# Kernel optimization log

Measured on AMD Instinct MI355X. Metric: run time of the kernel, lower is better.

Reference implementation:

```python
import jax, jax.numpy as jnp
import numpy as np

N_KW = 65536
N_DOC = 65536
N = N_KW + N_DOC
D_NODE = 128   # kw_size == middle_dim
D_MID = 128
D_FB = 16
D_T = 8
E = 1048576


def setup_inputs() -> dict:
    key = jax.random.key(0)
    ks = jax.random.split(key, 14)
    X_nodes = jax.random.normal(ks[0], (N, D_NODE), jnp.float32)
    X_feedback = jax.random.normal(ks[1], (N_DOC, D_FB), jnp.float32)
    X_time = jax.random.normal(ks[2], (N_DOC, D_T), jnp.float32)
    src = jax.random.randint(ks[3], (E,), 0, N_KW)            # kw node ids
    dst = N_KW + jax.random.randint(ks[4], (E,), 0, N_DOC)    # doc node ids
    edge_kw2doc = jnp.stack([src, dst])                       # [2, E], row0=src
    edge_doc2kw = jnp.stack([dst, src])

    def lin(k, fan_in, fan_out):
        return jax.random.normal(k, (fan_in, fan_out), jnp.float32) / np.sqrt(fan_in).astype(np.float32)

    params = dict(
        W0=lin(ks[5], D_NODE, D_MID), b0=jnp.zeros((D_MID,), jnp.float32),
        Wg1=lin(ks[6], D_MID, D_MID), bg1=jnp.zeros((D_MID,), jnp.float32),
        Wg2=lin(ks[7], D_MID, D_MID), bg2=jnp.zeros((D_MID,), jnp.float32),
        Wf1=lin(ks[8], D_FB, D_MID), bf1=jnp.zeros((D_MID,), jnp.float32),
        Wf2=lin(ks[9], D_MID, D_MID), bf2=jnp.zeros((D_MID,), jnp.float32),
        Wt1=lin(ks[10], D_T, D_MID), bt1=jnp.zeros((D_MID,), jnp.float32),
        Wt2=lin(ks[11], D_MID, D_MID), bt2=jnp.zeros((D_MID,), jnp.float32),
    )
    return {"X_nodes": X_nodes, "X_feedback": X_feedback, "X_time": X_time,
            "edge_kw2doc": edge_kw2doc, "edge_doc2kw": edge_doc2kw, "n_kw": N_KW, **params}


def _gcn(x, edge, W, b, n):
    # PyG GCNConv: add self-loops, symmetric normalization deg^{-1/2} A deg^{-1/2}, then linear.
    loop = jnp.arange(n)
    srcs = jnp.concatenate([edge[0], loop])
    dsts = jnp.concatenate([edge[1], loop])
    deg = jax.ops.segment_sum(jnp.ones(srcs.shape[0], x.dtype), dsts, num_segments=n)
    dis = jnp.where(deg > 0, jax.lax.rsqrt(jnp.maximum(deg, 1e-12)), jnp.zeros((), x.dtype))
    norm = dis[srcs] * dis[dsts]
    h = x @ W                                   # [N, D_MID]
    msg = h[srcs] * norm[:, None]               # gather on src, [E+N, D_MID]
    return jax.ops.segment_sum(msg, dsts, num_segments=n) + b


def reference(X_nodes, X_feedback, X_time, edge_kw2doc, edge_doc2kw, n_kw,
              W0, b0, Wg1, bg1, Wg2, bg2, Wf1, bf1, Wf2, bf2, Wt1, bt1, Wt2, bt2):
    n = X_nodes.shape[0]
    # feedback / time MLPs (relu on all but last layer)
    xf = jax.nn.relu(X_feedback @ Wf1 + bf1) @ Wf2 + bf2   # [N_DOC, D_MID]
    xt = jax.nn.relu(X_time @ Wt1 + bt1) @ Wt2 + bt2       # [N_DOC, D_MID]
    # layer 0: Linear on kw nodes only; doc rows stay zero
    x = jnp.zeros((n, W0.shape[1]), X_nodes.dtype)
    x = x.at[:n_kw].set(jax.nn.relu(X_nodes[:n_kw] @ W0 + b0))
    # layer 1: GCNConv kw2doc, write doc rows
    x2 = jax.nn.relu(_gcn(x, edge_kw2doc, Wg1, bg1, n))
    x = x.at[n_kw:].set(x2[n_kw:])
    # layer 2: GCNConv doc2kw, write kw rows
    x2 = jax.nn.relu(_gcn(x, edge_doc2kw, Wg2, bg2, n))
    x = x.at[:n_kw].set(x2[:n_kw])
    # merge_f (Mul) then merge_t (Mul) on doc rows
    x = x.at[n_kw:].mul(xf)
    x = x.at[n_kw:].mul(xt)
    return x
```

## Files before the change

kernel.cpp:

```cpp
#include <hip/hip_runtime.h>

#define NKW   65536
#define NDOC  65536
#define NSEG  131072
#define NE    1048576
#define CHUNK 4096
#define NBLK  (NE / CHUNK)

typedef unsigned long long u64;
typedef unsigned short     u16;
typedef unsigned int       u32;
typedef unsigned char      u8;

typedef __attribute__((ext_vector_type(8))) short short8;
typedef __attribute__((ext_vector_type(4))) float f32x4;
typedef __attribute__((ext_vector_type(2))) float f32x2;

union U8 { short8 v; u64 u[2]; short s[8]; };

__device__ __forceinline__ u16 f2bf(float f) {
    u32 u = __builtin_bit_cast(u32, f);
    u = (u + 0x7fffu + ((u >> 16) & 1u)) >> 16;
    return (u16)u;
}
__device__ __forceinline__ float bf2f(u16 h) {
    return __builtin_bit_cast(float, (u32)h << 16);
}
__device__ __forceinline__ u8 f2fp8(float f) {
    u32 pk = __builtin_amdgcn_cvt_pk_fp8_f32(f, f, 0u, false);
    return (u8)pk;
}

#define BUFA_OFF 0ull
#define BUFD_OFF 8388608ull
#define BUFB_OFF 16777216ull
#define BUFC_OFF 33554432ull
#define WF_OFF   50331648ull
#define CSR_OFF  51380224ull
#define CNT_OFF  59768832ull
#define AUX_OFF  60293120ull
#define OFF_OFF  60821504ull
#define DIS_OFF  61345792ull

#define WOFF_W0  0
#define WOFF_WG1 2048
#define WOFF_WG2 4096
#define WOFF_WF1 6144
#define WOFF_WF2 8192
#define WOFF_WT1 10240
#define WOFF_WT2 12288

struct PrepArgs { const float* w[7]; int K[7]; };

__global__ void zero_k(int* __restrict__ p) {
    p[blockIdx.x * 256 + threadIdx.x] = 0;
}

__global__ __launch_bounds__(256) void k1_hist_prep(
        const int* __restrict__ src, const int* __restrict__ dst,
        int* __restrict__ bhist, PrepArgs pa, short8* __restrict__ wfb) {
    __shared__ int h[512];
    const int tid = threadIdx.x;
    if (blockIdx.x < NBLK) {
        for (int i = tid; i < 512; i += 256) h[i] = 0;
        __syncthreads();
        int e0 = blockIdx.x * CHUNK;
        for (int i = tid; i < CHUNK; i += 256) {
            int s = src[e0 + i];
            int d = dst[e0 + i] - NKW;
            atomicAdd(&h[s >> 8], 1);
            atomicAdd(&h[256 + (d >> 8)], 1);
        }
        __syncthreads();
        for (int i = tid; i < 512; i += 256)
            if (h[i]) atomicAdd(&bhist[i], h[i]);
    } else {
        int u = (blockIdx.x - NBLK) * 4 + (tid >> 6);
        if (u < 224) {
            int m = u >> 5, bk = u & 31;
            int kc = bk >> 3, ct = bk & 7;
            int l = tid & 63;
            int K = pa.K[m];
            const float* W = pa.w[m];
            U8 o;
            #pragma unroll
            for (int i = 0; i < 8; ++i) {
                int k   = kc * 32 + 4 * (l >> 4) + (i & 3) + 16 * (i >> 2);
                int col = ct * 16 + (l & 15);
                float v = (k < K) ? W[(size_t)k * 128 + col] : 0.f;
                o.s[i] = (short)f2bf(v);
            }
            wfb[(size_t)m * 2048 + bk * 64 + l] = o.v;
        }
    }
}

__global__ __launch_bounds__(256) void k2_part_gates(
        const int* __restrict__ src, const int* __restrict__ dst,
        const int* __restrict__ bhist, int* __restrict__ bfill,
        u32* __restrict__ pairs,
        const short8* __restrict__ wfb,
        const float* __restrict__ Xfb, const float* __restrict__ Xt,
        const float* __restrict__ bf1v, const float* __restrict__ bf2v,
        const float* __restrict__ bt1v, const float* __restrict__ bt2v,
        u16* __restrict__ g) {
    __shared__ int h[512], sc[512], base[512], gb[512];
    __shared__ u32 staged[2 * CHUNK];
    const int tid = threadIdx.x;

    if (blockIdx.x < NBLK) {
        for (int i = tid; i < 512; i += 256) gb[i] = bhist[i];
        __syncthreads();
        for (int d = 1; d < 512; d <<= 1) {
            int i1 = tid + 256;
            int t0 = (tid >= d) ? gb[tid - d] : 0;
            int t1 = gb[i1 - d];
            __syncthreads();
            gb[tid] += t0; gb[i1] += t1;
            __syncthreads();
        }
        for (int i = tid; i < 512; i += 256) gb[i] -= bhist[i];
        for (int i = tid; i < 512; i += 256) h[i] = 0;
        __syncthreads();

        const int e0 = blockIdx.x * CHUNK;
        int se[16], de[16];
        #pragma unroll
        for (int j = 0; j < 16; ++j) {
            int e = e0 + tid + j * 256;
            se[j] = src[e];
            de[j] = dst[e] - NKW;
            atomicAdd(&h[se[j] >> 8], 1);
            atomicAdd(&h[256 + (de[j] >> 8)], 1);
        }
        __syncthreads();

        sc[tid] = h[tid];
        __syncthreads();
        for (int d = 1; d < 256; d <<= 1) {
            int t = (tid >= d) ? sc[tid - d] : 0;
            __syncthreads();
            sc[tid] += t;
            __syncthreads();
        }
        sc[256 + tid] = h[256 + tid];
        __syncthreads();
        for (int d = 1; d < 256; d <<= 1) {
            int t = (tid >= d) ? sc[256 + tid - d] : 0;
            __syncthreads();
            sc[256 + tid] += t;
            __syncthreads();
        }

        for (int i = tid; i < 512; i += 256) {
            base[i] = gb[i] + atomicAdd(&bfill[i], h[i]);
            sc[i] -= h[i];
            h[i] = 0;
        }
        __syncthreads();

        #pragma unroll
        for (int j = 0; j < 16; ++j) {
            int bk = se[j] >> 8;
            int r  = atomicAdd(&h[bk], 1);
            staged[sc[bk] + r] = ((u32)(se[j] & 255) << 16) | (u32)de[j];
            int bd = 256 + (de[j] >> 8);
            int r2 = atomicAdd(&h[bd], 1);
            staged[CHUNK + sc[bd] + r2] = ((u32)(de[j] & 255) << 16) | (u32)se[j];
        }
        __syncthreads();

        for (int i = tid; i < 512; i += 256) {
            int n = h[i];
            int so = (i < 256 ? 0 : CHUNK) + sc[i];
            u32* dp = pairs + base[i];
            for (int j = 0; j < n; ++j) dp[j] = staged[so + j];
        }
        return;
    }

    u16 (*H)[136] = (u16(*)[136])staged;
    const int w = tid >> 6, l = tid & 63, lr = l & 15, q = l >> 4;
    const int blk  = blockIdx.x - NBLK;
    const int row0 = blk * 64 + w * 16;
    const int lrow = w * 16 + lr;
    const int orow = w * 16 + 4 * q;

    f32x4 acc[8];
    {
        U8 a;
        f32x4 x = *(const f32x4*)(Xfb + (size_t)(row0 + lr) * 16 + 4 * q);
        #pragma unroll
        for (int i = 0; i < 4; ++i) { a.s[i] = (short)f2bf(x[i]); a.s[4 + i] = 0; }
        #pragma unroll
        for (int ct = 0; ct < 8; ++ct)
            acc[ct] = __builtin_amdgcn_mfma_f32_16x16x32_bf16(
                          a.v, wfb[WOFF_WF1 + ct * 64 + l], (f32x4){0.f,0.f,0.f,0.f}, 0, 0, 0);
    }
    #pragma unroll
    for (int ct = 0; ct < 8; ++ct) {
        const int col = ct * 16 + lr;
        const float bb = bf1v[col];
        #pragma unroll
        for (int r = 0; r < 4; ++r)
            H[orow + r][col] = f2bf(fmaxf(acc[ct][r] + bb, 0.f));
    }
    __threadfence_block();

    f32x4 accf[8];
    #pragma unroll
    for (int ct = 0; ct < 8; ++ct) accf[ct] = (f32x4){0.f, 0.f, 0.f, 0.f};
    #pragma unroll
    for (int kc = 0; kc < 4; ++kc) {
        U8 a;
        const int kb = kc * 32 + 4 * q;
        a.u[0] = *(const u64*)&H[lrow][kb];
        a.u[1] = *(const u64*)&H[lrow][kb + 16];
        #pragma unroll
        for (int ct = 0; ct < 8; ++ct)
            accf[ct] = __builtin_amdgcn_mfma_f32_16x16x32_bf16(
                           a.v, wfb[WOFF_WF2 + (kc * 8 + ct) * 64 + l], accf[ct], 0, 0, 0);
    }
    __threadfence_block();

    {
        U8 a;
        #pragma unroll
        for (int i = 0; i < 8; ++i) a.s[i] = 0;
        if (q < 2) {
            f32x4 x = *(const f32x4*)(Xt + (size_t)(row0 + lr) * 8 + 4 * q);
            #pragma unroll
            for (int i = 0; i < 4; ++i) a.s[i] = (short)f2bf(x[i]);
        }
        #pragma unroll
        for (int ct = 0; ct < 8; ++ct)
            acc[ct] = __builtin_amdgcn_mfma_f32_16x16x32_bf16(
                          a.v, wfb[WOFF_WT1 + ct * 64 + l], (f32x4){0.f,0.f,0.f,0.f}, 0, 0, 0);
    }
    #pragma unroll
    for (int ct = 0; ct < 8; ++ct) {
        const int col = ct * 16 + lr;
        const float bb = bt1v[col];
        #pragma unroll
        for (int r = 0; r < 4; ++r)
            H[orow + r][col] = f2bf(fmaxf(acc[ct][r] + bb, 0.f));
    }
    __threadfence_block();

    f32x4 acct[8];
    #pragma unroll
    for (int ct = 0; ct < 8; ++ct) acct[ct] = (f32x4){0.f, 0.f, 0.f, 0.f};
    #pragma unroll
    for (int kc = 0; kc < 4; ++kc) {
        U8 a;
        const int kb = kc * 32 + 4 * q;
        a.u[0] = *(const u64*)&H[lrow][kb];
        a.u[1] = *(const u64*)&H[lrow][kb + 16];
        #pragma unroll
        for (int ct = 0; ct < 8; ++ct)
            acct[ct] = __builtin_amdgcn_mfma_f32_16x16x32_bf16(
                           a.v, wfb[WOFF_WT2 + (kc * 8 + ct) * 64 + l], acct[ct], 0, 0, 0);
    }
    #pragma unroll
    for (int ct = 0; ct < 8; ++ct) {
        const int col = ct * 16 + lr;
        const float b2f = bf2v[col];
        const float b2t = bt2v[col];
        #pragma unroll
        for (int r = 0; r < 4; ++r) {
            float gv = (accf[ct][r] + b2f) * (acct[ct][r] + b2t);
            g[(size_t)(blk * 64 + orow + r) * 128 + col] = f2bf(gv);
        }
    }
}

__global__ __launch_bounds__(256) void k3_build_gemm0(
        const u32* __restrict__ pairs, const int* __restrict__ bhist,
        int* __restrict__ off, int* __restrict__ cnt,
        float* __restrict__ dis, int* __restrict__ csr,
        const float* __restrict__ Xn, const short8* __restrict__ wfb,
        const float* __restrict__ b0, u8* __restrict__ h0f8) {
    __shared__ int lcnt[256], loff[256], bs[256], gsc[512];
    const int tid = threadIdx.x;

    if (blockIdx.x < 512) {
        const int b = blockIdx.x;
        for (int i = tid; i < 512; i += 256) gsc[i] = bhist[i];
        __syncthreads();
        for (int d = 1; d < 512; d <<= 1) {
            int i1 = tid + 256;
            int t0 = (tid >= d) ? gsc[tid - d] : 0;
            int t1 = gsc[i1 - d];
            __syncthreads();
            gsc[tid] += t0; gsc[i1] += t1;
            __syncthreads();
        }
        const int size  = bhist[b];
        const int start = gsc[b] - size;
        lcnt[tid] = 0;
        __syncthreads();
        for (int i = tid; i < size; i += 256)
            atomicAdd(&lcnt[(pairs[start + i] >> 16) & 255], 1);
        __syncthreads();
        int s = lcnt[tid];
        bs[tid] = s;
        __syncthreads();
        for (int d = 1; d < 256; d <<= 1) {
            int t = (tid >= d) ? bs[tid - d] : 0;
            __syncthreads();
            bs[tid] += t;
            __syncthreads();
        }
        const int P = bs[tid] - s;
        const int seg = (b < 256) ? (b * 256 + tid) : (NKW + (b - 256) * 256 + tid);
        off[seg] = start + P;
        cnt[seg] = s;
        dis[seg] = rsqrtf((float)(s + 1));
        loff[tid] = P;
        lcnt[tid] = 0;
        __syncthreads();
        for (int i = tid; i < size; i += 256) {
            u32 p = pairs[start + i];
            int key = (p >> 16) & 255;
            int r = atomicAdd(&lcnt[key], 1);
            csr[start + loff[key] + r] = (int)(p & 0xFFFF);
        }
        return;
    }

    const int blk = blockIdx.x - 512;
    const int w = tid >> 6, l = tid & 63, lr = l & 15, q = l >> 4;
    const int row = blk * 64 + w * 16 + lr;
    f32x4 acc[8];
    #pragma unroll
    for (int ct = 0; ct < 8; ++ct) acc[ct] = (f32x4){0.f, 0.f, 0.f, 0.f};
    #pragma unroll
    for (int kc = 0; kc < 4; ++kc) {
        U8 a;
        const int kb = kc * 32 + 4 * q;
        const float* A = Xn + (size_t)row * 128;
        f32x4 lo = *(const f32x4*)(A + kb);
        f32x4 hi = *(const f32x4*)(A + kb + 16);
        #pragma unroll
        for (int i = 0; i < 4; ++i) {
            a.s[i]     = (short)f2bf(lo[i]);
            a.s[4 + i] = (short)f2bf(hi[i]);
        }
        #pragma unroll
        for (int ct = 0; ct < 8; ++ct)
            acc[ct] = __builtin_amdgcn_mfma_f32_16x16x32_bf16(
                          a.v, wfb[WOFF_W0 + (kc * 8 + ct) * 64 + l], acc[ct], 0, 0, 0);
    }
    const int orow0 = blk * 64 + w * 16 + 4 * q;
    #pragma unroll
    for (int ct = 0; ct < 8; ++ct) {
        const int col = ct * 16 + lr;
        const float bb = b0[col];
        #pragma unroll
        for (int r = 0; r < 4; ++r) {
            float v = fmaxf(acc[ct][r] + bb, 0.f);
            h0f8[(size_t)(orow0 + r) * 128 + col] = f2fp8(v);
        }
    }
}

template<bool KW_SIDE>
__global__ __launch_bounds__(256) void aggf8_k(
        const int* __restrict__ off, const int* __restrict__ cnt,
        const int* __restrict__ csr, const u8* __restrict__ gsrc,
        const u8* __restrict__ h0f8, const float* __restrict__ dis,
        u16* __restrict__ outb) {
    const int r    = blockIdx.x * 16 + (threadIdx.x >> 4);
    const int lane = threadIdx.x & 15;
    const int seg  = KW_SIDE ? r : (NKW + r);
    const int st = off[seg];
    const int n  = cnt[seg];
    float a[8];
    #pragma unroll
    for (int j = 0; j < 8; ++j) a[j] = 0.f;

    #define DECACC(vv) { \
        u32 lo_ = (u32)(vv), hi_ = (u32)((vv) >> 32); \
        f32x2 p0 = __builtin_amdgcn_cvt_pk_f32_fp8(lo_, false); \
        f32x2 p1 = __builtin_amdgcn_cvt_pk_f32_fp8(lo_, true);  \
        f32x2 p2 = __builtin_amdgcn_cvt_pk_f32_fp8(hi_, false); \
        f32x2 p3 = __builtin_amdgcn_cvt_pk_f32_fp8(hi_, true);  \
        a[0] += p0[0]; a[1] += p0[1]; a[2] += p1[0]; a[3] += p1[1]; \
        a[4] += p2[0]; a[5] += p2[1]; a[6] += p3[0]; a[7] += p3[1]; }

    int i = 0;
    for (; i + 8 <= n; i += 8) {
        int nb[8];
        #pragma unroll
        for (int k = 0; k < 8; ++k) nb[k] = csr[st + i + k];
        u64 v[8];
        #pragma unroll
        for (int k = 0; k < 8; ++k)
            v[k] = *(const u64*)(gsrc + (size_t)nb[k] * 128 + lane * 8);
        #pragma unroll
        for (int k = 0; k < 8; ++k) DECACC(v[k])
    }
    for (; i < n; ++i) {
        int nb = csr[st + i];
        u64 v = *(const u64*)(gsrc + (size_t)nb * 128 + lane * 8);
        DECACC(v)
    }
    #undef DECACC

    const float dk = dis[seg];
    if (KW_SIDE) {
        u64 hv = *(const u64*)(h0f8 + (size_t)r * 128 + lane * 8);
        u32 lo_ = (u32)hv, hi_ = (u32)(hv >> 32);
        f32x2 p0 = __builtin_amdgcn_cvt_pk_f32_fp8(lo_, false);
        f32x2 p1 = __builtin_amdgcn_cvt_pk_f32_fp8(lo_, true);
        f32x2 p2 = __builtin_amdgcn_cvt_pk_f32_fp8(hi_, false);
        f32x2 p3 = __builtin_amdgcn_cvt_pk_f32_fp8(hi_, true);
        float hh[8] = {p0[0], p0[1], p1[0], p1[1], p2[0], p2[1], p3[0], p3[1]};
        #pragma unroll
        for (int j = 0; j < 8; ++j) a[j] = dk * (a[j] + dk * hh[j]);
    } else {
        #pragma unroll
        for (int j = 0; j < 8; ++j) a[j] *= dk;
    }
    U8 o;
    #pragma unroll
    for (int j = 0; j < 8; ++j) o.s[j] = (short)f2bf(a[j]);
    *(short8*)(outb + (size_t)r * 128 + lane * 8) = o.v;
}

__global__ __launch_bounds__(256) void k7_gemm1g(
        const u16* __restrict__ aggin, const short8* __restrict__ wfb,
        const float* __restrict__ bg1, const u16* __restrict__ gmul,
        u8* __restrict__ xdocf8, float* __restrict__ outdoc) {
    const int tid = threadIdx.x;
    const int w = tid >> 6, l = tid & 63, lr = l & 15, q = l >> 4;
    const int row = blockIdx.x * 64 + w * 16 + lr;
    f32x4 acc[8];
    #pragma unroll
    for (int ct = 0; ct < 8; ++ct) acc[ct] = (f32x4){0.f, 0.f, 0.f, 0.f};
    #pragma unroll
    for (int kc = 0; kc < 4; ++kc) {
        U8 a;
        const int kb = kc * 32 + 4 * q;
        const u16* A = aggin + (size_t)row * 128;
        a.u[0] = *(const u64*)(A + kb);
        a.u[1] = *(const u64*)(A + kb + 16);
        #pragma unroll
        for (int ct = 0; ct < 8; ++ct)
            acc[ct] = __builtin_amdgcn_mfma_f32_16x16x32_bf16(
                          a.v, wfb[WOFF_WG1 + (kc * 8 + ct) * 64 + l], acc[ct], 0, 0, 0);
    }
    const int orow0 = blockIdx.x * 64 + w * 16 + 4 * q;
    #pragma unroll
    for (int ct = 0; ct < 8; ++ct) {
        const int col = ct * 16 + lr;
        const float bb = bg1[col];
        #pragma unroll
        for (int r = 0; r < 4; ++r) {
            float v = fmaxf(acc[ct][r] + bb, 0.f);
            const size_t idx = (size_t)(orow0 + r) * 128 + col;
            xdocf8[idx] = f2fp8(v);
            float o = v * bf2f(gmul[idx]);
            __builtin_nontemporal_store(o, outdoc + idx);
        }
    }
}

__global__ __launch_bounds__(256) void k8_gemm2(
        const u16* __restrict__ Av, const short8* __restrict__ wfb,
        const float* __restrict__ bg2, float* __restrict__ outf32) {
    const int tid = threadIdx.x;
    const int w = tid >> 6, l = tid & 63, lr = l & 15, q = l >> 4;
    const int row = blockIdx.x * 64 + w * 16 + lr;
    f32x4 acc[8];
    #pragma unroll
    for (int ct = 0; ct < 8; ++ct) acc[ct] = (f32x4){0.f, 0.f, 0.f, 0.f};
    #pragma unroll
    for (int kc = 0; kc < 4; ++kc) {
        U8 a;
        const int kb = kc * 32 + 4 * q;
        const u16* A = Av + (size_t)row * 128;
        a.u[0] = *(const u64*)(A + kb);
        a.u[1] = *(const u64*)(A + kb + 16);
        #pragma unroll
        for (int ct = 0; ct < 8; ++ct)
            acc[ct] = __builtin_amdgcn_mfma_f32_16x16x32_bf16(
                          a.v, wfb[WOFF_WG2 + (kc * 8 + ct) * 64 + l], acc[ct], 0, 0, 0);
    }
    const int orow0 = blockIdx.x * 64 + w * 16 + 4 * q;
    #pragma unroll
    for (int ct = 0; ct < 8; ++ct) {
        const int col = ct * 16 + lr;
        const float bb = bg2[col];
        #pragma unroll
        for (int r = 0; r < 4; ++r) {
            float v = fmaxf(acc[ct][r] + bb, 0.f);
            __builtin_nontemporal_store(v, outf32 + (size_t)(orow0 + r) * 128 + col);
        }
    }
}

extern "C" void kernel_launch(void* const* d_in, const int* in_sizes, int n_in,
                              void* d_out, int out_size, void* d_ws, size_t ws_size,
                              hipStream_t stream) {
    const float* Xn  = (const float*)d_in[0];
    const float* Xfb = (const float*)d_in[1];
    const float* Xt  = (const float*)d_in[2];
    const int*   e01 = (const int*)d_in[3];
    const float* W0  = (const float*)d_in[6];
    const float* b0  = (const float*)d_in[7];
    const float* Wg1 = (const float*)d_in[8];
    const float* bg1 = (const float*)d_in[9];
    const float* Wg2 = (const float*)d_in[10];
    const float* bg2 = (const float*)d_in[11];
    const float* Wf1 = (const float*)d_in[12];
    const float* bf1 = (const float*)d_in[13];
    const float* Wf2 = (const float*)d_in[14];
    const float* bf2 = (const float*)d_in[15];
    const float* Wt1 = (const float*)d_in[16];
    const float* bt1 = (const float*)d_in[17];
    const float* Wt2 = (const float*)d_in[18];
    const float* bt2 = (const float*)d_in[19];

    float* out = (float*)d_out;
    char*  ws  = (char*)d_ws;
    u8*    bufA  = (u8*)(ws + BUFA_OFF);
    u8*    bufD  = (u8*)(ws + BUFD_OFF);
    u16*   bufB  = (u16*)(ws + BUFB_OFF);
    u16*   bufC  = (u16*)(ws + BUFC_OFF);
    u32*   pairs = (u32*)(ws + BUFC_OFF);
    short8* wfb  = (short8*)(ws + WF_OFF);
    int*   csr   = (int*)(ws + CSR_OFF);
    int*   cnt   = (int*)(ws + CNT_OFF);
    int*   bhist = (int*)(ws + AUX_OFF);
    int*   bfill = bhist + 512;
    int*   off   = (int*)(ws + OFF_OFF);
    float* dis   = (float*)(ws + DIS_OFF);

    const int* src = e01;
    const int* dst = e01 + NE;

    PrepArgs pa;
    pa.w[0] = W0;  pa.K[0] = 128;
    pa.w[1] = Wg1; pa.K[1] = 128;
    pa.w[2] = Wg2; pa.K[2] = 128;
    pa.w[3] = Wf1; pa.K[3] = 16;
    pa.w[4] = Wf2; pa.K[4] = 128;
    pa.w[5] = Wt1; pa.K[5] = 8;
    pa.w[6] = Wt2; pa.K[6] = 128;

    zero_k<<<4, 256, 0, stream>>>(bhist);
    k1_hist_prep<<<NBLK + 56, 256, 0, stream>>>(src, dst, bhist, pa, wfb);
    k2_part_gates<<<NBLK + 1024, 256, 0, stream>>>(
        src, dst, bhist, bfill, pairs,
        wfb, Xfb, Xt, bf1, bf2, bt1, bt2, bufB);
    k3_build_gemm0<<<512 + 1024, 256, 0, stream>>>(
        pairs, bhist, off, cnt, dis, csr, Xn, wfb, b0, bufA);

    aggf8_k<false><<<NDOC / 16, 256, 0, stream>>>(off, cnt, csr, bufA, nullptr, dis, bufC);
    k7_gemm1g<<<1024, 256, 0, stream>>>(bufC, wfb, bg1, bufB, bufD,
                                        out + (size_t)NKW * 128);

    aggf8_k<true><<<NKW / 16, 256, 0, stream>>>(off, cnt, csr, bufD, bufA, dis, bufC);
    k8_gemm2<<<1024, 256, 0, stream>>>(bufC, wfb, bg2, out);
}
```

Baseline: 155.8 us.

## Split feedback/time MLP gate across partition and CSR-build kernels

The gate MLPs (feedback and time) were computed entirely inside the partition kernel's extra blocks. They are now split into two stages. The first-layer hidden activations are computed by separate blocks in k2 and written to two new bf16 global buffers. The second-layer GEMMs and the gate product are computed by extra blocks in k3, alongside the CSR build and GEMM0. This spreads the MFMA work across two kernels to balance load against the partition and scatter blocks. The cost is writing and re-reading two 16 MB intermediate buffers through global memory.

```diff
diff --git a/kernel.cpp b/kernel.cpp
--- a/kernel.cpp
+++ b/kernel.cpp
@@ -41,6 +41,8 @@
 #define AUX_OFF  60293120ull
 #define OFF_OFF  60821504ull
 #define DIS_OFF  61345792ull
+#define BUFE_OFF 67108864ull
+#define BUFF_OFF 83886080ull
 
 #define WOFF_W0  0
 #define WOFF_WG1 2048
@@ -95,15 +97,14 @@
     }
 }
 
-__global__ __launch_bounds__(256) void k2_part_gates(
+__global__ __launch_bounds__(256) void k2_part_s1(
         const int* __restrict__ src, const int* __restrict__ dst,
         const int* __restrict__ bhist, int* __restrict__ bfill,
         u32* __restrict__ pairs,
         const short8* __restrict__ wfb,
         const float* __restrict__ Xfb, const float* __restrict__ Xt,
-        const float* __restrict__ bf1v, const float* __restrict__ bf2v,
-        const float* __restrict__ bt1v, const float* __restrict__ bt2v,
-        u16* __restrict__ g) {
+        const float* __restrict__ bf1v, const float* __restrict__ bt1v,
+        u16* __restrict__ hidf, u16* __restrict__ hidt) {
     __shared__ int h[512], sc[512], base[512], gb[512];
     __shared__ u32 staged[2 * CHUNK];
     const int tid = threadIdx.x;
@@ -179,107 +180,67 @@
         return;
     }
 
-    u16 (*H)[136] = (u16(*)[136])staged;
     const int w = tid >> 6, l = tid & 63, lr = l & 15, q = l >> 4;
-    const int blk  = blockIdx.x - NBLK;
-    const int row0 = blk * 64 + w * 16;
-    const int lrow = w * 16 + lr;
-    const int orow = w * 16 + 4 * q;
-
     f32x4 acc[8];
-    {
+    #pragma unroll
+    for (int ct = 0; ct < 8; ++ct) acc[ct] = (f32x4){0.f, 0.f, 0.f, 0.f};
+
+    if (blockIdx.x < NBLK + 1024) {
+        const int blk = blockIdx.x - NBLK;
+        const int row = blk * 64 + w * 16 + lr;
         U8 a;
-        f32x4 x = *(const f32x4*)(Xfb + (size_t)(row0 + lr) * 16 + 4 * q);
+        f32x4 x = *(const f32x4*)(Xfb + (size_t)row * 16 + 4 * q);
         #pragma unroll
         for (int i = 0; i < 4; ++i) { a.s[i] = (short)f2bf(x[i]); a.s[4 + i] = 0; }
         #pragma unroll
         for (int ct = 0; ct < 8; ++ct)
             acc[ct] = __builtin_amdgcn_mfma_f32_16x16x32_bf16(
-                          a.v, wfb[WOFF_WF1 + ct * 64 + l], (f32x4){0.f,0.f,0.f,0.f}, 0, 0, 0);
-    }
-    #pragma unroll
-    for (int ct = 0; ct < 8; ++ct) {
-        const int col = ct * 16 + lr;
-        const float bb = bf1v[col];
-        #pragma unroll
-        for (int r = 0; r < 4; ++r)
-            H[orow + r][col] = f2bf(fmaxf(acc[ct][r] + bb, 0.f));
-    }
-    __threadfence_block();
-
-    f32x4 accf[8];
-    #pragma unroll
-    for (int ct = 0; ct < 8; ++ct) accf[ct] = (f32x4){0.f, 0.f, 0.f, 0.f};
-    #pragma unroll
-    for (int kc = 0; kc < 4; ++kc) {
-        U8 a;
-        const int kb = kc * 32 + 4 * q;
-        a.u[0] = *(const u64*)&H[lrow][kb];
-        a.u[1] = *(const u64*)&H[lrow][kb + 16];
-        #pragma unroll
-        for (int ct = 0; ct < 8; ++ct)
-            accf[ct] = __builtin_amdgcn_mfma_f32_16x16x32_bf16(
-                           a.v, wfb[WOFF_WF2 + (kc * 8 + ct) * 64 + l], accf[ct], 0, 0, 0);
-    }
-    __threadfence_block();
-
-    {
+                          a.v, wfb[WOFF_WF1 + ct * 64 + l], acc[ct], 0, 0, 0);
+        const int orow0 = blk * 64 + w * 16 + 4 * q;
+        #pragma unroll
+        for (int ct = 0; ct < 8; ++ct) {
+            const int col = ct * 16 + lr;
+            const float bb = bf1v[col];
+            #pragma unroll
+            for (int r = 0; r < 4; ++r)
+                hidf[(size_t)(orow0 + r) * 128 + col] = f2bf(fmaxf(acc[ct][r] + bb, 0.f));
+        }
+    } else {
+        const int blk = blockIdx.x - NBLK - 1024;
+        const int row = blk * 64 + w * 16 + lr;
         U8 a;
         #pragma unroll
         for (int i = 0; i < 8; ++i) a.s[i] = 0;
         if (q < 2) {
-            f32x4 x = *(const f32x4*)(Xt + (size_t)(row0 + lr) * 8 + 4 * q);
+            f32x4 x = *(const f32x4*)(Xt + (size_t)row * 8 + 4 * q);
             #pragma unroll
             for (int i = 0; i < 4; ++i) a.s[i] = (short)f2bf(x[i]);
         }
         #pragma unroll
         for (int ct = 0; ct < 8; ++ct)
             acc[ct] = __builtin_amdgcn_mfma_f32_16x16x32_bf16(
-                          a.v, wfb[WOFF_WT1 + ct * 64 + l], (f32x4){0.f,0.f,0.f,0.f}, 0, 0, 0);
-    }
-    #pragma unroll
-    for (int ct = 0; ct < 8; ++ct) {
-        const int col = ct * 16 + lr;
-        const float bb = bt1v[col];
-        #pragma unroll
-        for (int r = 0; r < 4; ++r)
-            H[orow + r][col] = f2bf(fmaxf(acc[ct][r] + bb, 0.f));
-    }
-    __threadfence_block();
-
-    f32x4 acct[8];
-    #pragma unroll
-    for (int ct = 0; ct < 8; ++ct) acct[ct] = (f32x4){0.f, 0.f, 0.f, 0.f};
-    #pragma unroll
-    for (int kc = 0; kc < 4; ++kc) {
-        U8 a;
-        const int kb = kc * 32 + 4 * q;
-        a.u[0] = *(const u64*)&H[lrow][kb];
-        a.u[1] = *(const u64*)&H[lrow][kb + 16];
-        #pragma unroll
-        for (int ct = 0; ct < 8; ++ct)
-            acct[ct] = __builtin_amdgcn_mfma_f32_16x16x32_bf16(
-                           a.v, wfb[WOFF_WT2 + (kc * 8 + ct) * 64 + l], acct[ct], 0, 0, 0);
-    }
-    #pragma unroll
-    for (int ct = 0; ct < 8; ++ct) {
-        const int col = ct * 16 + lr;
-        const float b2f = bf2v[col];
-        const float b2t = bt2v[col];
-        #pragma unroll
-        for (int r = 0; r < 4; ++r) {
-            float gv = (accf[ct][r] + b2f) * (acct[ct][r] + b2t);
-            g[(size_t)(blk * 64 + orow + r) * 128 + col] = f2bf(gv);
-        }
-    }
-}
-
-__global__ __launch_bounds__(256) void k3_build_gemm0(
+                          a.v, wfb[WOFF_WT1 + ct * 64 + l], acc[ct], 0, 0, 0);
+        const int orow0 = blk * 64 + w * 16 + 4 * q;
+        #pragma unroll
+        for (int ct = 0; ct < 8; ++ct) {
+            const int col = ct * 16 + lr;
+            const float bb = bt1v[col];
+            #pragma unroll
+            for (int r = 0; r < 4; ++r)
+                hidt[(size_t)(orow0 + r) * 128 + col] = f2bf(fmaxf(acc[ct][r] + bb, 0.f));
+        }
+    }
+}
+
+__global__ __launch_bounds__(256) void k3_build_gemm0_s2(
         const u32* __restrict__ pairs, const int* __restrict__ bhist,
         int* __restrict__ off, int* __restrict__ cnt,
         float* __restrict__ dis, int* __restrict__ csr,
         const float* __restrict__ Xn, const short8* __restrict__ wfb,
-        const float* __restrict__ b0, u8* __restrict__ h0f8) {
+        const float* __restrict__ b0, u8* __restrict__ h0f8,
+        const u16* __restrict__ hidf, const u16* __restrict__ hidt,
+        const float* __restrict__ bf2v, const float* __restrict__ bt2v,
+        u16* __restrict__ g) {
     __shared__ int lcnt[256], loff[256], bs[256], gsc[512];
     const int tid = threadIdx.x;
 
@@ -328,38 +289,82 @@
         return;
     }
 
-    const int blk = blockIdx.x - 512;
     const int w = tid >> 6, l = tid & 63, lr = l & 15, q = l >> 4;
+
+    if (blockIdx.x < 1536) {
+        const int blk = blockIdx.x - 512;
+        const int row = blk * 64 + w * 16 + lr;
+        f32x4 acc[8];
+        #pragma unroll
+        for (int ct = 0; ct < 8; ++ct) acc[ct] = (f32x4){0.f, 0.f, 0.f, 0.f};
+        #pragma unroll
+        for (int kc = 0; kc < 4; ++kc) {
+            U8 a;
+            const int kb = kc * 32 + 4 * q;
+            const float* A = Xn + (size_t)row * 128;
+            f32x4 lo = *(const f32x4*)(A + kb);
+            f32x4 hi = *(const f32x4*)(A + kb + 16);
+            #pragma unroll
+            for (int i = 0; i < 4; ++i) {
+                a.s[i]     = (short)f2bf(lo[i]);
+                a.s[4 + i] = (short)f2bf(hi[i]);
+            }
+            #pragma unroll
+            for (int ct = 0; ct < 8; ++ct)
+                acc[ct] = __builtin_amdgcn_mfma_f32_16x16x32_bf16(
+                              a.v, wfb[WOFF_W0 + (kc * 8 + ct) * 64 + l], acc[ct], 0, 0, 0);
+        }
+        const int orow0 = blk * 64 + w * 16 + 4 * q;
+        #pragma unroll
+        for (int ct = 0; ct < 8; ++ct) {
+            const int col = ct * 16 + lr;
+            const float bb = b0[col];
+            #pragma unroll
+            for (int r = 0; r < 4; ++r) {
+                float v = fmaxf(acc[ct][r] + bb, 0.f);
+                h0f8[(size_t)(orow0 + r) * 128 + col] = f2fp8(v);
+            }
+        }
+        return;
+    }
+
+    const int blk = blockIdx.x - 1536;
     const int row = blk * 64 + w * 16 + lr;
-    f32x4 acc[8];
-    #pragma unroll
-    for (int ct = 0; ct < 8; ++ct) acc[ct] = (f32x4){0.f, 0.f, 0.f, 0.f};
+    f32x4 accf[8], acct[8];
+    #pragma unroll
+    for (int ct = 0; ct < 8; ++ct) {
+        accf[ct] = (f32x4){0.f, 0.f, 0.f, 0.f};
+        acct[ct] = (f32x4){0.f, 0.f, 0.f, 0.f};
+    }
     #pragma unroll
     for (int kc = 0; kc < 4; ++kc) {
+        const int kb = kc * 32 + 4 * q;
         U8 a;
-        const int kb = kc * 32 + 4 * q;
-        const float* A = Xn + (size_t)row * 128;
-        f32x4 lo = *(const f32x4*)(A + kb);
-        f32x4 hi = *(const f32x4*)(A + kb + 16);
-        #pragma unroll
-        for (int i = 0; i < 4; ++i) {
-            a.s[i]     = (short)f2bf(lo[i]);
-            a.s[4 + i] = (short)f2bf(hi[i]);
-        }
+        const u16* Af = hidf + (size_t)row * 128;
+        a.u[0] = *(const u64*)(Af + kb);
+        a.u[1] = *(const u64*)(Af + kb + 16);
         #pragma unroll
         for (int ct = 0; ct < 8; ++ct)
-            acc[ct] = __builtin_amdgcn_mfma_f32_16x16x32_bf16(
-                          a.v, wfb[WOFF_W0 + (kc * 8 + ct) * 64 + l], acc[ct], 0, 0, 0);
+            accf[ct] = __builtin_amdgcn_mfma_f32_16x16x32_bf16(
+                           a.v, wfb[WOFF_WF2 + (kc * 8 + ct) * 64 + l], accf[ct], 0, 0, 0);
+        const u16* At = hidt + (size_t)row * 128;
+        a.u[0] = *(const u64*)(At + kb);
+        a.u[1] = *(const u64*)(At + kb + 16);
+        #pragma unroll
+        for (int ct = 0; ct < 8; ++ct)
+            acct[ct] = __builtin_amdgcn_mfma_f32_16x16x32_bf16(
+                           a.v, wfb[WOFF_WT2 + (kc * 8 + ct) * 64 + l], acct[ct], 0, 0, 0);
     }
     const int orow0 = blk * 64 + w * 16 + 4 * q;
     #pragma unroll
     for (int ct = 0; ct < 8; ++ct) {
         const int col = ct * 16 + lr;
-        const float bb = b0[col];
+        const float b2f = bf2v[col];
+        const float b2t = bt2v[col];
         #pragma unroll
         for (int r = 0; r < 4; ++r) {
-            float v = fmaxf(acc[ct][r] + bb, 0.f);
-            h0f8[(size_t)(orow0 + r) * 128 + col] = f2fp8(v);
+            float gv = (accf[ct][r] + b2f) * (acct[ct][r] + b2t);
+            g[(size_t)(orow0 + r) * 128 + col] = f2bf(gv);
         }
     }
 }
@@ -536,6 +541,8 @@
     int*   bfill = bhist + 512;
     int*   off   = (int*)(ws + OFF_OFF);
     float* dis   = (float*)(ws + DIS_OFF);
+    u16*   bufE  = (u16*)(ws + BUFE_OFF);
+    u16*   bufF  = (u16*)(ws + BUFF_OFF);
 
     const int* src = e01;
     const int* dst = e01 + NE;
@@ -551,11 +558,12 @@
 
     zero_k<<<4, 256, 0, stream>>>(bhist);
     k1_hist_prep<<<NBLK + 56, 256, 0, stream>>>(src, dst, bhist, pa, wfb);
-    k2_part_gates<<<NBLK + 1024, 256, 0, stream>>>(
+    k2_part_s1<<<NBLK + 2048, 256, 0, stream>>>(
         src, dst, bhist, bfill, pairs,
-        wfb, Xfb, Xt, bf1, bf2, bt1, bt2, bufB);
-    k3_build_gemm0<<<512 + 1024, 256, 0, stream>>>(
-        pairs, bhist, off, cnt, dis, csr, Xn, wfb, b0, bufA);
+        wfb, Xfb, Xt, bf1, bt1, bufE, bufF);
+    k3_build_gemm0_s2<<<512 + 2048, 256, 0, stream>>>(
+        pairs, bhist, off, cnt, dis, csr, Xn, wfb, b0, bufA,
+        bufE, bufF, bf2, bt2, bufB);
 
     aggf8_k<false><<<NDOC / 16, 256, 0, stream>>>(off, cnt, csr, bufA, nullptr, dis, bufC);
     k7_gemm1g<<<1024, 256, 0, stream>>>(bufC, wfb, bg1, bufB, bufD,
```

After: 159.3 us. 1.02x slower.
